# Kernel optimization log

Hardware: AMD Instinct MI355X
Metric: run time of the kernel (lower is better)

## Reference

```python
import jax, jax.numpy as jnp
import numpy as np

B, S, H = 2, 1024, 1024      # batch, seq, hidden_size
FF = 4096                     # shared-expert intermediate_size
E, K, M = 64, 8, 512          # num_experts, top_k, moe_intermediate_size


def setup_inputs() -> dict:
    key = jax.random.key(0)
    ks = jax.random.split(key, 6)
    f32 = jnp.float32
    return {
        "hidden_states": jax.random.normal(ks[0], (B, S, H), f32),
        "Ws1": jax.random.normal(ks[1], (H, FF), f32) * (1.0 / np.sqrt(H)),
        "Ws2": jax.random.normal(ks[2], (FF, H), f32) * (1.0 / np.sqrt(FF)),
        "Wg":  jax.random.normal(ks[3], (H, E), f32) * (1.0 / np.sqrt(H)),
        "W1":  jax.random.normal(ks[4], (E, H, M), f32) * (1.0 / np.sqrt(H)),
        "W2":  jax.random.normal(ks[5], (E, M, H), f32) * (1.0 / np.sqrt(M)),
    }


def reference(hidden_states, Ws1, Ws2, Wg, W1, W2):
    b, s, h = hidden_states.shape
    x = hidden_states.reshape(b * s, h)                 # [T, H]

    # shared expert: SiLU-MLP applied to every token
    shared = jax.nn.silu(x @ Ws1) @ Ws2                 # [T, H]

    # router: top-k gating, softmax over the selected logits only
    logits = x @ Wg                                     # [T, E]
    vals, idx = jax.lax.top_k(logits, K)                # [T, K]
    rw = jax.nn.softmax(vals, axis=-1)                  # [T, K]
    # combine[t, e] = routing weight of expert e for token t (0 if unselected)
    combine = (jax.nn.one_hot(idx, E, dtype=x.dtype) * rw[..., None]).sum(axis=1)  # [T, E]

    # per-expert dense FFN, weighted scatter-add combine (scan keeps memory at O(T*H))
    def step(acc, ew):
        w1, w2, c = ew                                  # [H,M], [M,H], [T]
        y = jax.nn.silu(x @ w1) @ w2                    # [T, H]
        return acc + c[:, None] * y, None

    expert_out, _ = jax.lax.scan(step, jnp.zeros_like(x), (W1, W2, combine.T))

    out = (shared + expert_out).reshape(b, s, h)
    return out, logits.reshape(b, s, E)
```

## Files before the change

kernel.cpp:

```cpp
#include <hip/hip_runtime.h>
#include <cmath>


typedef _Float16 f16;
typedef __attribute__((ext_vector_type(4))) _Float16 f16x4;
typedef __attribute__((ext_vector_type(8))) _Float16 f16x8;
typedef __attribute__((ext_vector_type(4))) float f32x4;

#define NT 2048
#define HD 1024
#define FF 4096
#define NE 64
#define TOPK 8
#define MD 512

constexpr size_t SZ_H1 = (size_t)NT * FF * 2;
constexpr size_t SZ_HX = (size_t)(NT * TOPK + 128) * MD * 2;
constexpr size_t O_H1 = 0;
constexpr size_t O_HX = O_H1 + SZ_H1;
constexpr size_t O_TOPKI = O_HX + SZ_HX;
constexpr size_t O_TOPKW = O_TOPKI + (size_t)NT * TOPK * 4;
constexpr size_t O_COUNTS = O_TOPKW + (size_t)NT * TOPK * 4;
constexpr size_t O_CURSORS = O_COUNTS + 256;
constexpr size_t O_OFFSETS = O_CURSORS + 256;
constexpr size_t O_RTOK = O_OFFSETS + 256;
constexpr size_t O_RW = O_RTOK + (size_t)NT * TOPK * 4;
constexpr size_t O_TSLOT = O_RW + (size_t)NT * TOPK * 4;
constexpr size_t O_XH = ((O_TSLOT + (size_t)NT * TOPK * 4 + 255) / 256) * 256;
constexpr size_t O_W1T = O_XH + (size_t)NT * HD * 2;
constexpr size_t O_W2T = O_W1T + (size_t)NE * HD * MD * 2;
constexpr size_t O_WS1T = O_W2T + (size_t)NE * MD * HD * 2;
constexpr size_t O_WS2T = O_WS1T + (size_t)HD * FF * 2;
constexpr size_t O_HY = O_WS2T + (size_t)FF * HD * 2;
constexpr size_t SZ_HY = (size_t)(NT * TOPK + 128) * HD * 2;
constexpr size_t O_S2P = O_HY + SZ_HY;
constexpr size_t WS_NEEDED = O_S2P + (size_t)4 * NT * HD * 4;

__device__ __forceinline__ void lds16(void* l, const void* g) {
    __builtin_amdgcn_global_load_lds(
        (const __attribute__((address_space(1))) void*)g,
        (__attribute__((address_space(3))) void*)l, 16, 0, 0);
}

__global__ __launch_bounds__(256) void k_router(const float* __restrict__ X,
                                                const float* __restrict__ Wg,
                                                float* __restrict__ logits)
{
    __shared__ float xs[4][HD];
    const int tid = threadIdx.x;
    const int t0 = blockIdx.x * 4;
    #pragma unroll
    for (int i = 0; i < 4; ++i) {
        int f4 = tid + i * 256;
        int row = f4 >> 8;
        int col = (f4 & 255) * 4;
        *(float4*)&xs[row][col] = *(const float4*)&X[(t0 + row) * HD + col];
    }
    __syncthreads();
    const int e = tid & 63, tok = tid >> 6;
    float a0 = 0.f, a1 = 0.f, a2 = 0.f, a3 = 0.f;
    const float* xr = xs[tok];
    for (int h = 0; h < HD; h += 4) {
        a0 += xr[h + 0] * Wg[(h + 0) * NE + e];
        a1 += xr[h + 1] * Wg[(h + 1) * NE + e];
        a2 += xr[h + 2] * Wg[(h + 2) * NE + e];
        a3 += xr[h + 3] * Wg[(h + 3) * NE + e];
    }
    logits[(t0 + tok) * NE + e] = (a0 + a1) + (a2 + a3);
}

__global__ __launch_bounds__(64) void k_topk(const float* __restrict__ logits,
                                             int* __restrict__ topk_idx,
                                             float* __restrict__ topk_w,
                                             int* __restrict__ counts)
{
    const int t = blockIdx.x;
    const int lane = threadIdx.x;
    __shared__ float sval[TOPK];
    __shared__ int sidx[TOPK];
    float cur = logits[t * NE + lane];
    for (int it = 0; it < TOPK; ++it) {
        float v = cur; int id = lane;
        #pragma unroll
        for (int off = 32; off > 0; off >>= 1) {
            float ov = __shfl_xor(v, off, 64);
            int   oi = __shfl_xor(id, off, 64);
            if (ov > v || (ov == v && oi < id)) { v = ov; id = oi; }
        }
        if (lane == 0) { sval[it] = v; sidx[it] = id; }
        if (lane == id) cur = -INFINITY;
    }
    __syncthreads();
    if (lane < TOPK) {
        float m = sval[0];
        float denom = 0.f;
        #pragma unroll
        for (int j = 0; j < TOPK; ++j) denom += expf(sval[j] - m);
        float w = expf(sval[lane] - m) / denom;
        int e = sidx[lane];
        topk_idx[t * TOPK + lane] = e;
        topk_w[t * TOPK + lane] = w;
        atomicAdd(&counts[e], 1);
    }
}

__global__ void k_scan(const int* __restrict__ counts, int* __restrict__ offsets)
{
    if (threadIdx.x == 0) {
        int run = 0;
        for (int e = 0; e < NE; ++e) { offsets[e] = run; run += counts[e]; }
    }
}

__global__ __launch_bounds__(256) void k_route(const int* __restrict__ topk_idx,
                                               const float* __restrict__ topk_w,
                                               const int* __restrict__ offsets,
                                               int* __restrict__ cursors,
                                               int* __restrict__ rtok,
                                               int* __restrict__ tslot)
{
    int i = blockIdx.x * 256 + threadIdx.x;
    int e = topk_idx[i];
    int pos = atomicAdd(&cursors[e], 1);
    int slot = offsets[e] + pos;
    rtok[slot] = i >> 3;
    tslot[i] = slot;
}

__global__ __launch_bounds__(256) void k_cvt_x(const float* __restrict__ X,
                                               f16* __restrict__ Xh)
{
    int i = blockIdx.x * 256 + threadIdx.x;
    float4 v = ((const float4*)X)[i];
    f16x4 h = { (f16)v.x, (f16)v.y, (f16)v.z, (f16)v.w };
    ((f16x4*)Xh)[i] = h;
}

__global__ __launch_bounds__(256) void k_cvt_t(const float* __restrict__ src,
                                               f16* __restrict__ dst,
                                               int K, int N)
{
    const size_t bofs = (size_t)blockIdx.z * K * N;
    src += bofs; dst += bofs;
    const int n0 = blockIdx.x * 64, k0 = blockIdx.y * 64;
    __shared__ f16 t[64][68];
    const int tid = threadIdx.x;
    #pragma unroll
    for (int i = 0; i < 4; ++i) {
        int idx = tid + i * 256;
        int r = idx >> 4, c4 = (idx & 15) * 4;
        float4 v = *(const float4*)&src[(size_t)(k0 + r) * N + n0 + c4];
        f16x4 h = { (f16)v.x, (f16)v.y, (f16)v.z, (f16)v.w };
        *(f16x4*)&t[r][c4] = h;
    }
    __syncthreads();
    #pragma unroll
    for (int i = 0; i < 4; ++i) {
        int idx = tid + i * 256;
        int nr = idx >> 4, kc = (idx & 15) * 4;
        f16x4 o = { t[kc][nr], t[kc + 1][nr], t[kc + 2][nr], t[kc + 3][nr] };
        *(f16x4*)&dst[(size_t)(n0 + nr) * K + k0 + kc] = o;
    }
}


#define GEMM_PREAMBLE                                                        \
    const int tid = threadIdx.x, lane = tid & 63, wave = tid >> 6;           \
    const int wm = (wave >> 1) * 64, wn = (wave & 1) * 64;                   \
    const int fr = lane & 15, q = lane >> 4;                                 \
    const int qs = (q ^ ((fr >> 1) & 3)) * 8;                                \
    const int sr = lane >> 2;                                                \
    const int sc = ((lane & 3) ^ ((lane >> 3) & 3)) * 8;

#define GEMM_LDS                                                             \
    __shared__ alignas(16) f16 As[3][128 * 32];                              \
    __shared__ alignas(16) f16 Bs[3][128 * 32];

#define GEMM_STAGE(si, ofs)                                                  \
    lds16(&As[si][wave * 32 * 32], gA0 + (ofs));                             \
    lds16(&As[si][(wave * 32 + 16) * 32], gA1 + (ofs));                      \
    lds16(&Bs[si][wave * 32 * 32], gB0 + (ofs));                             \
    lds16(&Bs[si][(wave * 32 + 16) * 32], gB1 + (ofs));

#define GEMM_MFMA(ri)                                                        \
    {                                                                        \
        f16x8 af[4], bf[4];                                                  \
        _Pragma("unroll")                                                    \
        for (int i = 0; i < 4; ++i)                                          \
            af[i] = *(const f16x8*)&As[ri][(wm + i * 16 + fr) * 32 + qs];    \
        _Pragma("unroll")                                                    \
        for (int j = 0; j < 4; ++j)                                          \
            bf[j] = *(const f16x8*)&Bs[ri][(wn + j * 16 + fr) * 32 + qs];    \
        _Pragma("unroll")                                                    \
        for (int i = 0; i < 4; ++i)                                          \
            _Pragma("unroll")                                                \
            for (int j = 0; j < 4; ++j)                                      \
                acc[i][j] = __builtin_amdgcn_mfma_f32_16x16x32_f16(          \
                    af[i], bf[j], acc[i][j], 0, 0, 0);                       \
    }

#define GEMM_LOOP(KITERS)                                                    \
    GEMM_STAGE(0, 0)                                                         \
    GEMM_STAGE(1, 32)                                                        \
    _Pragma("unroll")                                                        \
    for (int t = 0; t < (KITERS); ++t) {                                     \
        if (t < (KITERS) - 1)                                                \
            asm volatile("s_waitcnt vmcnt(4)" ::: "memory");                 \
        else                                                                 \
            asm volatile("s_waitcnt vmcnt(0)" ::: "memory");                 \
        __builtin_amdgcn_s_barrier();                                        \
        asm volatile("" ::: "memory");                                       \
        if (t + 2 < (KITERS)) { GEMM_STAGE((t + 2) % 3, (t + 2) * 32) }      \
        GEMM_MFMA(t % 3)                                                     \
    }

__global__ __launch_bounds__(256) void g_shared1(const f16* __restrict__ Xh,
                                                 const f16* __restrict__ Bt,
                                                 f16* __restrict__ H1)
{
    GEMM_LDS
    GEMM_PREAMBLE
    const int m0 = blockIdx.y * 128, n0 = blockIdx.x * 128;
    const f16* gA0 = Xh + (size_t)(m0 + wave * 32 + sr) * HD + sc;
    const f16* gA1 = gA0 + (size_t)16 * HD;
    const f16* gB0 = Bt + (size_t)(n0 + wave * 32 + sr) * HD + sc;
    const f16* gB1 = gB0 + (size_t)16 * HD;

    f32x4 acc[4][4] = {};
    GEMM_LOOP(32)

    #pragma unroll
    for (int i = 0; i < 4; ++i)
        #pragma unroll
        for (int j = 0; j < 4; ++j)
            #pragma unroll
            for (int r = 0; r < 4; ++r) {
                int m = m0 + wm + i * 16 + q * 4 + r;
                int n = n0 + wn + j * 16 + fr;
                float v = acc[i][j][r];
                H1[(size_t)m * FF + n] = (f16)(v / (1.f + expf(-v)));
            }
}

__global__ __launch_bounds__(256) void g_shared2(const f16* __restrict__ H1,
                                                 const f16* __restrict__ Bt,
                                                 float* __restrict__ S2p)
{
    GEMM_LDS
    GEMM_PREAMBLE
    const int m0 = blockIdx.y * 128, n0 = blockIdx.x * 128;
    const int kbase = blockIdx.z * (FF / 4);
    float* P = S2p + (size_t)blockIdx.z * NT * HD;
    const f16* gA0 = H1 + (size_t)(m0 + wave * 32 + sr) * FF + kbase + sc;
    const f16* gA1 = gA0 + (size_t)16 * FF;
    const f16* gB0 = Bt + (size_t)(n0 + wave * 32 + sr) * FF + kbase + sc;
    const f16* gB1 = gB0 + (size_t)16 * FF;

    f32x4 acc[4][4] = {};
    GEMM_LOOP(32)

    #pragma unroll
    for (int i = 0; i < 4; ++i)
        #pragma unroll
        for (int j = 0; j < 4; ++j)
            #pragma unroll
            for (int r = 0; r < 4; ++r) {
                int m = m0 + wm + i * 16 + q * 4 + r;
                int n = n0 + wn + j * 16 + fr;
                P[(size_t)m * HD + n] = acc[i][j][r];
            }
}

__global__ __launch_bounds__(256) void g_exp1(const f16* __restrict__ Xh,
                                              const f16* __restrict__ W1t,
                                              const int* __restrict__ counts,
                                              const int* __restrict__ offsets,
                                              const int* __restrict__ rtok,
                                              f16* __restrict__ Hx)
{
    const int lid = blockIdx.x;
    const int rres = lid & 7;
    const int t2 = lid >> 3;
    const int k = t2 & 63;
    const int g = t2 >> 6;
    const int e = g * 8 + rres;
    const int cnt = counts[e];
    const int mt = (k >> 2) * 128;
    if (mt >= cnt) return;
    const int off = offsets[e];
    const int n0 = (k & 3) * 128;
    const f16* W = W1t + (size_t)e * MD * HD;

    GEMM_LDS
    GEMM_PREAMBLE

    int rm0 = mt + wave * 32 + sr;
    int rm1 = rm0 + 16;
    int s0 = off + (rm0 < cnt ? rm0 : cnt - 1);
    int s1 = off + (rm1 < cnt ? rm1 : cnt - 1);
    const f16* gA0 = Xh + (size_t)rtok[s0] * HD + sc;
    const f16* gA1 = Xh + (size_t)rtok[s1] * HD + sc;
    const f16* gB0 = W + (size_t)(n0 + wave * 32 + sr) * HD + sc;
    const f16* gB1 = gB0 + (size_t)16 * HD;

    f32x4 acc[4][4] = {};
    GEMM_LOOP(32)

    #pragma unroll
    for (int i = 0; i < 4; ++i)
        #pragma unroll
        for (int j = 0; j < 4; ++j)
            #pragma unroll
            for (int r = 0; r < 4; ++r) {
                int m_in = mt + wm + i * 16 + q * 4 + r;
                if (m_in < cnt) {
                    int n = n0 + wn + j * 16 + fr;
                    float v = acc[i][j][r];
                    Hx[(size_t)(off + m_in) * MD + n] = (f16)(v / (1.f + expf(-v)));
                }
            }
}

__global__ __launch_bounds__(256) void g_exp2(const f16* __restrict__ Hx,
                                              const f16* __restrict__ W2t,
                                              const int* __restrict__ counts,
                                              const int* __restrict__ offsets,
                                              f16* __restrict__ Hy)
{
    const int lid = blockIdx.x;
    const int rres = lid & 7;
    const int t2 = lid >> 3;
    const int k = t2 & 127;
    const int g = t2 >> 7;
    const int e = g * 8 + rres;
    const int cnt = counts[e];
    const int mt = (k >> 3) * 128;
    if (mt >= cnt) return;
    const int off = offsets[e];
    const int n0 = (k & 7) * 128;
    const f16* W = W2t + (size_t)e * HD * MD;

    GEMM_LDS
    GEMM_PREAMBLE

    const f16* gA0 = Hx + (size_t)(off + mt + wave * 32 + sr) * MD + sc;
    const f16* gA1 = gA0 + (size_t)16 * MD;
    const f16* gB0 = W + (size_t)(n0 + wave * 32 + sr) * MD + sc;
    const f16* gB1 = gB0 + (size_t)16 * MD;

    f32x4 acc[4][4] = {};
    GEMM_LOOP(16)

    #pragma unroll
    for (int i = 0; i < 4; ++i)
        #pragma unroll
        for (int j = 0; j < 4; ++j)
            #pragma unroll
            for (int r = 0; r < 4; ++r) {
                int m_in = mt + wm + i * 16 + q * 4 + r;
                if (m_in < cnt) {
                    int n = n0 + wn + j * 16 + fr;
                    Hy[(size_t)(off + m_in) * HD + n] = (f16)acc[i][j][r];
                }
            }
}

__global__ __launch_bounds__(256) void k_gather(const float* __restrict__ S2p,
                                                const f16* __restrict__ Hy,
                                                const int* __restrict__ tslot,
                                                const float* __restrict__ tw,
                                                float* __restrict__ Out)
{
    const int t = blockIdx.x;
    const int tid = threadIdx.x;
    __shared__ int ss[TOPK];
    __shared__ float sw[TOPK];
    if (tid < TOPK) {
        ss[tid] = tslot[t * TOPK + tid];
        sw[tid] = tw[t * TOPK + tid];
    }
    __syncthreads();
    const int h = tid * 4;
    float4 a = *(const float4*)&S2p[(size_t)t * HD + h];
    #pragma unroll
    for (int z = 1; z < 4; ++z) {
        float4 b = *(const float4*)&S2p[(size_t)z * NT * HD + (size_t)t * HD + h];
        a.x += b.x; a.y += b.y; a.z += b.z; a.w += b.w;
    }
    #pragma unroll
    for (int kk = 0; kk < TOPK; ++kk) {
        f16x4 y = *(const f16x4*)&Hy[(size_t)ss[kk] * HD + h];
        float w = sw[kk];
        a.x += w * (float)y[0];
        a.y += w * (float)y[1];
        a.z += w * (float)y[2];
        a.w += w * (float)y[3];
    }
    *(float4*)&Out[(size_t)t * HD + h] = a;
}

extern "C" void kernel_launch(void* const* d_in, const int* in_sizes, int n_in,
                              void* d_out, int out_size, void* d_ws, size_t ws_size,
                              hipStream_t stream)
{
    (void)in_sizes; (void)n_in; (void)out_size; (void)ws_size;
    const float* X   = (const float*)d_in[0];
    const float* Ws1 = (const float*)d_in[1];
    const float* Ws2 = (const float*)d_in[2];
    const float* Wg  = (const float*)d_in[3];
    const float* W1  = (const float*)d_in[4];
    const float* W2  = (const float*)d_in[5];
    float* out = (float*)d_out;
    float* logits = out + (size_t)NT * HD;

    char* ws = (char*)d_ws;
    f16*   h1       = (f16*)(ws + O_H1);
    f16*   hx       = (f16*)(ws + O_HX);
    int*   topk_idx = (int*)(ws + O_TOPKI);
    float* topk_w   = (float*)(ws + O_TOPKW);
    int*   counts   = (int*)(ws + O_COUNTS);
    int*   cursors  = (int*)(ws + O_CURSORS);
    int*   offsets  = (int*)(ws + O_OFFSETS);
    int*   rtok     = (int*)(ws + O_RTOK);
    int*   tslot    = (int*)(ws + O_TSLOT);
    f16*   xh       = (f16*)(ws + O_XH);
    f16*   w1t      = (f16*)(ws + O_W1T);
    f16*   w2t      = (f16*)(ws + O_W2T);
    f16*   ws1t     = (f16*)(ws + O_WS1T);
    f16*   ws2t     = (f16*)(ws + O_WS2T);
    f16*   hy       = (f16*)(ws + O_HY);
    float* s2p      = (float*)(ws + O_S2P);

    hipMemsetAsync(counts, 0, 512, stream);

    k_router<<<NT / 4, 256, 0, stream>>>(X, Wg, logits);
    k_topk<<<NT, 64, 0, stream>>>(logits, topk_idx, topk_w, counts);
    k_scan<<<1, 64, 0, stream>>>(counts, offsets);
    k_route<<<NT * TOPK / 256, 256, 0, stream>>>(topk_idx, topk_w, offsets, cursors, rtok, tslot);

    k_cvt_x<<<NT * HD / 1024, 256, 0, stream>>>(X, xh);
    k_cvt_t<<<dim3(FF / 64, HD / 64, 1), 256, 0, stream>>>(Ws1, ws1t, HD, FF);
    k_cvt_t<<<dim3(HD / 64, FF / 64, 1), 256, 0, stream>>>(Ws2, ws2t, FF, HD);
    k_cvt_t<<<dim3(MD / 64, HD / 64, NE), 256, 0, stream>>>(W1, w1t, HD, MD);
    k_cvt_t<<<dim3(HD / 64, MD / 64, NE), 256, 0, stream>>>(W2, w2t, MD, HD);

    g_shared1<<<dim3(FF / 128, NT / 128), 256, 0, stream>>>(xh, ws1t, h1);
    g_shared2<<<dim3(HD / 128, NT / 128, 4), 256, 0, stream>>>(h1, ws2t, s2p);
    g_exp1<<<4096, 256, 0, stream>>>(xh, w1t, counts, offsets, rtok, hx);
    g_exp2<<<8192, 256, 0, stream>>>(hx, w2t, counts, offsets, hy);
    k_gather<<<NT, 256, 0, stream>>>(s2p, hy, tslot, topk_w, out);
}
```

Measured before the change: 612.4 us.

## Fuse expert weight fp32-to-fp16 conversion into expert GEMM B-tile loads

Removes the separate transpose/convert passes over the 64 expert W1 and W2 tensors. The expert GEMMs now read the fp32 weights directly, convert each B tile in registers and write it into swizzled LDS. A new pipelined loop overlaps the A-tile async LDS loads with the register-staged B loads. This avoids a full read and write of about 128 MB of fp32 expert weights per call. In exchange, weights are re-read as fp32 by every M-tile block that touches an expert, the per-lane loads are scalar and strided, and the loop waits on vmcnt(0) every iteration.

```diff
diff --git a/kernel.cpp b/kernel.cpp
--- a/kernel.cpp
+++ b/kernel.cpp
@@ -24,12 +24,9 @@
 constexpr size_t O_CURSORS = O_COUNTS + 256;
 constexpr size_t O_OFFSETS = O_CURSORS + 256;
 constexpr size_t O_RTOK = O_OFFSETS + 256;
-constexpr size_t O_RW = O_RTOK + (size_t)NT * TOPK * 4;
-constexpr size_t O_TSLOT = O_RW + (size_t)NT * TOPK * 4;
+constexpr size_t O_TSLOT = O_RTOK + (size_t)NT * TOPK * 4;
 constexpr size_t O_XH = ((O_TSLOT + (size_t)NT * TOPK * 4 + 255) / 256) * 256;
-constexpr size_t O_W1T = O_XH + (size_t)NT * HD * 2;
-constexpr size_t O_W2T = O_W1T + (size_t)NE * HD * MD * 2;
-constexpr size_t O_WS1T = O_W2T + (size_t)NE * MD * HD * 2;
+constexpr size_t O_WS1T = O_XH + (size_t)NT * HD * 2;
 constexpr size_t O_WS2T = O_WS1T + (size_t)HD * FF * 2;
 constexpr size_t O_HY = O_WS2T + (size_t)FF * HD * 2;
 constexpr size_t SZ_HY = (size_t)(NT * TOPK + 128) * HD * 2;
@@ -113,7 +110,6 @@
 }
 
 __global__ __launch_bounds__(256) void k_route(const int* __restrict__ topk_idx,
-                                               const float* __restrict__ topk_w,
                                                const int* __restrict__ offsets,
                                                int* __restrict__ cursors,
                                                int* __restrict__ rtok,
@@ -140,8 +136,6 @@
                                                f16* __restrict__ dst,
                                                int K, int N)
 {
-    const size_t bofs = (size_t)blockIdx.z * K * N;
-    src += bofs; dst += bofs;
     const int n0 = blockIdx.x * 64, k0 = blockIdx.y * 64;
     __shared__ f16 t[64][68];
     const int tid = threadIdx.x;
@@ -214,6 +208,56 @@
         GEMM_MFMA(t % 3)                                                     \
     }
 
+#define EXP_B_PREAMBLE(N0, LDBV)                                             \
+    const int bn = (N0) + wave * 32 + (lane & 31);                           \
+    const int bkh = lane >> 5;                                               \
+    const int brow = wave * 32 + (lane & 31);                                \
+    const int bxor = (brow >> 1) & 3;                                        \
+    const int ldb = (LDBV);                                                  \
+    float bw[16];
+
+#define EXP_ISSUE_B(krow)                                                    \
+    _Pragma("unroll")                                                        \
+    for (int kk = 0; kk < 16; ++kk)                                          \
+        bw[kk] = gW[(size_t)((krow) + bkh * 16 + kk) * ldb + bn];
+
+#define EXP_WRITE_B(si)                                                      \
+    {                                                                        \
+        f16x8 h0, h1;                                                        \
+        _Pragma("unroll")                                                    \
+        for (int kk = 0; kk < 8; ++kk) {                                     \
+            h0[kk] = (f16)bw[kk];                                            \
+            h1[kk] = (f16)bw[kk + 8];                                        \
+        }                                                                    \
+        *(f16x8*)&Bs[si][brow * 32 + ((bkh * 2 + 0) ^ bxor) * 8] = h0;       \
+        *(f16x8*)&Bs[si][brow * 32 + ((bkh * 2 + 1) ^ bxor) * 8] = h1;       \
+    }
+
+#define EXP_ISSUE_A(si, ofs)                                                 \
+    lds16(&As[si][wave * 32 * 32], gA0 + (ofs));                             \
+    lds16(&As[si][(wave * 32 + 16) * 32], gA1 + (ofs));
+
+#define GEMM_LOOP_WB(KITERS)                                                 \
+    EXP_ISSUE_A(0, 0)                                                        \
+    EXP_ISSUE_B(0)                                                           \
+    asm volatile("s_waitcnt vmcnt(0)" ::: "memory");                         \
+    EXP_WRITE_B(0)                                                           \
+    EXP_ISSUE_A(1, 32)                                                       \
+    EXP_ISSUE_B(32)                                                          \
+    _Pragma("unroll")                                                        \
+    for (int t = 0; t < (KITERS); ++t) {                                     \
+        asm volatile("s_waitcnt vmcnt(0)" ::: "memory");                     \
+        if (t + 1 < (KITERS)) { EXP_WRITE_B((t + 1) % 3) }                   \
+        asm volatile("s_waitcnt lgkmcnt(0)" ::: "memory");                   \
+        __builtin_amdgcn_s_barrier();                                        \
+        asm volatile("" ::: "memory");                                       \
+        if (t + 2 < (KITERS)) {                                              \
+            EXP_ISSUE_A((t + 2) % 3, (t + 2) * 32)                           \
+            EXP_ISSUE_B((t + 2) * 32)                                        \
+        }                                                                    \
+        GEMM_MFMA(t % 3)                                                     \
+    }
+
 __global__ __launch_bounds__(256) void g_shared1(const f16* __restrict__ Xh,
                                                  const f16* __restrict__ Bt,
                                                  f16* __restrict__ H1)
@@ -272,7 +316,7 @@
 }
 
 __global__ __launch_bounds__(256) void g_exp1(const f16* __restrict__ Xh,
-                                              const f16* __restrict__ W1t,
+                                              const float* __restrict__ W1,
                                               const int* __restrict__ counts,
                                               const int* __restrict__ offsets,
                                               const int* __restrict__ rtok,
@@ -289,10 +333,11 @@
     if (mt >= cnt) return;
     const int off = offsets[e];
     const int n0 = (k & 3) * 128;
-    const f16* W = W1t + (size_t)e * MD * HD;
+    const float* gW = W1 + (size_t)e * HD * MD;
 
     GEMM_LDS
     GEMM_PREAMBLE
+    EXP_B_PREAMBLE(n0, MD)
 
     int rm0 = mt + wave * 32 + sr;
     int rm1 = rm0 + 16;
@@ -300,11 +345,9 @@
     int s1 = off + (rm1 < cnt ? rm1 : cnt - 1);
     const f16* gA0 = Xh + (size_t)rtok[s0] * HD + sc;
     const f16* gA1 = Xh + (size_t)rtok[s1] * HD + sc;
-    const f16* gB0 = W + (size_t)(n0 + wave * 32 + sr) * HD + sc;
-    const f16* gB1 = gB0 + (size_t)16 * HD;
 
     f32x4 acc[4][4] = {};
-    GEMM_LOOP(32)
+    GEMM_LOOP_WB(32)
 
     #pragma unroll
     for (int i = 0; i < 4; ++i)
@@ -322,7 +365,7 @@
 }
 
 __global__ __launch_bounds__(256) void g_exp2(const f16* __restrict__ Hx,
-                                              const f16* __restrict__ W2t,
+                                              const float* __restrict__ W2,
                                               const int* __restrict__ counts,
                                               const int* __restrict__ offsets,
                                               f16* __restrict__ Hy)
@@ -338,18 +381,17 @@
     if (mt >= cnt) return;
     const int off = offsets[e];
     const int n0 = (k & 7) * 128;
-    const f16* W = W2t + (size_t)e * HD * MD;
+    const float* gW = W2 + (size_t)e * MD * HD;
 
     GEMM_LDS
     GEMM_PREAMBLE
+    EXP_B_PREAMBLE(n0, HD)
 
     const f16* gA0 = Hx + (size_t)(off + mt + wave * 32 + sr) * MD + sc;
     const f16* gA1 = gA0 + (size_t)16 * MD;
-    const f16* gB0 = W + (size_t)(n0 + wave * 32 + sr) * MD + sc;
-    const f16* gB1 = gB0 + (size_t)16 * MD;
 
     f32x4 acc[4][4] = {};
-    GEMM_LOOP(16)
+    GEMM_LOOP_WB(16)
 
     #pragma unroll
     for (int i = 0; i < 4; ++i)
@@ -424,8 +466,6 @@
     int*   rtok     = (int*)(ws + O_RTOK);
     int*   tslot    = (int*)(ws + O_TSLOT);
     f16*   xh       = (f16*)(ws + O_XH);
-    f16*   w1t      = (f16*)(ws + O_W1T);
-    f16*   w2t      = (f16*)(ws + O_W2T);
     f16*   ws1t     = (f16*)(ws + O_WS1T);
     f16*   ws2t     = (f16*)(ws + O_WS2T);
     f16*   hy       = (f16*)(ws + O_HY);
@@ -436,17 +476,15 @@
     k_router<<<NT / 4, 256, 0, stream>>>(X, Wg, logits);
     k_topk<<<NT, 64, 0, stream>>>(logits, topk_idx, topk_w, counts);
     k_scan<<<1, 64, 0, stream>>>(counts, offsets);
-    k_route<<<NT * TOPK / 256, 256, 0, stream>>>(topk_idx, topk_w, offsets, cursors, rtok, tslot);
+    k_route<<<NT * TOPK / 256, 256, 0, stream>>>(topk_idx, offsets, cursors, rtok, tslot);
 
     k_cvt_x<<<NT * HD / 1024, 256, 0, stream>>>(X, xh);
-    k_cvt_t<<<dim3(FF / 64, HD / 64, 1), 256, 0, stream>>>(Ws1, ws1t, HD, FF);
-    k_cvt_t<<<dim3(HD / 64, FF / 64, 1), 256, 0, stream>>>(Ws2, ws2t, FF, HD);
-    k_cvt_t<<<dim3(MD / 64, HD / 64, NE), 256, 0, stream>>>(W1, w1t, HD, MD);
-    k_cvt_t<<<dim3(HD / 64, MD / 64, NE), 256, 0, stream>>>(W2, w2t, MD, HD);
+    k_cvt_t<<<dim3(FF / 64, HD / 64), 256, 0, stream>>>(Ws1, ws1t, HD, FF);
+    k_cvt_t<<<dim3(HD / 64, FF / 64), 256, 0, stream>>>(Ws2, ws2t, FF, HD);
 
     g_shared1<<<dim3(FF / 128, NT / 128), 256, 0, stream>>>(xh, ws1t, h1);
     g_shared2<<<dim3(HD / 128, NT / 128, 4), 256, 0, stream>>>(h1, ws2t, s2p);
-    g_exp1<<<4096, 256, 0, stream>>>(xh, w1t, counts, offsets, rtok, hx);
-    g_exp2<<<8192, 256, 0, stream>>>(hx, w2t, counts, offsets, hy);
+    g_exp1<<<4096, 256, 0, stream>>>(xh, W1, counts, offsets, rtok, hx);
+    g_exp2<<<8192, 256, 0, stream>>>(hx, W2, counts, offsets, hy);
     k_gather<<<NT, 256, 0, stream>>>(s2p, hy, tslot, topk_w, out);
 }
```

Result: faster. 536.7 us (-12.4%).
